# Kernel optimization log

Hardware: AMD Instinct MI355X
Metric: run time of the kernel (lower is better)

## Reference

```python
import jax, jax.numpy as jnp
import numpy as np

B, C, H, W = 4, 8, 384, 384
NUM_LAYERS = 5
CG_ITERS = 10


def conv2d(x, w, b):
    # x: [B,Cin,H,W], w: [Cout,Cin,3,3]
    y = jax.lax.conv_general_dilated(x, w, (1, 1), 'SAME',
                                     dimension_numbers=('NCHW', 'OIHW', 'NCHW'))
    return y + b[None, :, None, None]


def dw(x, w_in, b_in, ws_mid, bs_mid, w_out, b_out):
    # Sequence: conv, conv, relu, conv, conv, relu, conv, conv, relu, conv, conv, relu, conv
    h = conv2d(x, w_in, b_in)
    for i in range(7):
        h = conv2d(h, ws_mid[i], bs_mid[i])
        if i % 2 == 0:  # ReLU after convs 2,4,6,8
            h = jax.nn.relu(h)
    h = conv2d(h, w_out, b_out)
    return x + h  # residual


def conjugate_grad(rhs, csm_c, mask, lam):
    # rhs: [B,H,W] complex; csm_c: [B,C,H,W] complex; mask: [B,H,W] real
    def AtA(p):
        coil = csm_c * p[:, None]                      # [B,C,H,W]
        k = jnp.fft.fft2(coil) * mask[:, None]         # masked k-space
        return jnp.sum(jnp.conj(csm_c) * jnp.fft.ifft2(k), axis=1)

    def body(carry, _):
        x, r, p, rTr = carry
        Ap = AtA(p) + lam * p
        pAp = jnp.sum(jnp.conj(p) * Ap, axis=(-2, -1)).real
        alpha = rTr / pAp
        x = x + alpha[:, None, None] * p
        r = r - alpha[:, None, None] * Ap
        rTrNew = jnp.sum(jnp.conj(r) * r, axis=(-2, -1)).real
        beta = rTrNew / rTr
        p = r + beta[:, None, None] * p
        return (x, r, p, rTrNew), None

    x0 = jnp.zeros_like(rhs)
    rTr0 = jnp.sum(jnp.conj(rhs) * rhs, axis=(-2, -1)).real
    (x, _, _, _), _ = jax.lax.scan(body, (x0, rhs, rhs, rTr0), None, length=CG_ITERS)
    return x


def reference(under_img, csm, mask, lam, w_in, b_in, ws_mid, bs_mid, w_out, b_out):
    csm_c = jax.lax.complex(csm[..., 0], csm[..., 1])  # [B,C,H,W] complex
    lam_s = lam[0]
    x = under_img
    for _ in range(NUM_LAYERS):
        x = dw(x, w_in, b_in, ws_mid, bs_mid, w_out, b_out)
        x = under_img + lam_s * x
        rhs = jax.lax.complex(x[:, 0], x[:, 1])        # view_as_complex(permute(0,2,3,1))
        xc = conjugate_grad(rhs, csm_c, mask, lam_s)
        x = jnp.stack([xc.real, xc.imag], axis=1)      # view_as_real -> [B,2,H,W]
    return x


def setup_inputs() -> dict:
    key = jax.random.key(0)
    ks = jax.random.split(key, 8)
    under_img = jax.random.normal(ks[0], (B, 2, H, W), jnp.float32)
    csm = jax.random.normal(ks[1], (B, C, H, W, 2), jnp.float32) / np.sqrt(C)
    mask = (jax.random.uniform(ks[2], (B, H, W)) > 0.5).astype(jnp.float32)
    lam = jnp.array([0.05], jnp.float32)
    w_in = jax.random.normal(ks[3], (64, 2, 3, 3), jnp.float32) * 0.02
    b_in = jnp.zeros((64,), jnp.float32)
    ws_mid = jax.random.normal(ks[4], (7, 64, 64, 3, 3), jnp.float32) * 0.02
    bs_mid = jnp.zeros((7, 64), jnp.float32)
    w_out = jax.random.normal(ks[5], (2, 64, 3, 3), jnp.float32) * 0.02
    b_out = jnp.zeros((2,), jnp.float32)
    return {"under_img": under_img, "csm": csm, "mask": mask, "lam": lam,
            "w_in": w_in, "b_in": b_in, "ws_mid": ws_mid, "bs_mid": bs_mid,
            "w_out": w_out, "b_out": b_out}
```

## Files before the change

kernel.cpp:

```cpp
#include <hip/hip_runtime.h>
#include <hip/hip_bf16.h>
#include <math.h>

#define HH 384
#define WW 384
#define HW (HH*WW)
#define WP 386
#define PP (386*386)
#define BB 4
#define CC 8
#define NLAYERS 5
#define CGITERS 10
#define PI_F 3.14159265358979323846f

typedef __attribute__((ext_vector_type(8))) short short8;
typedef __attribute__((ext_vector_type(4))) float floatx4;

struct cf { float x, y; };
__device__ __forceinline__ cf cadd(cf a, cf b){ cf r; r.x=a.x+b.x; r.y=a.y+b.y; return r; }
__device__ __forceinline__ cf csub(cf a, cf b){ cf r; r.x=a.x-b.x; r.y=a.y-b.y; return r; }
__device__ __forceinline__ cf cmul(cf a, cf b){ cf r; r.x=a.x*b.x - a.y*b.y; r.y=a.x*b.y + a.y*b.x; return r; }
__device__ __forceinline__ cf csqr(cf a){ cf r; r.x = a.x*a.x - a.y*a.y; r.y = 2.f*a.x*a.y; return r; }
__device__ __forceinline__ cf shflxor(cf v, int m){ cf r; r.x = __shfl_xor(v.x, m); r.y = __shfl_xor(v.y, m); return r; }
__device__ __forceinline__ int brev7(int l){ return (int)(__brev((unsigned)l) >> 25); }
__device__ __forceinline__ int padi(int i){ return i + (i >> 3); }

__device__ __forceinline__ void radix3(cf a0, cf a1, cf a2, float s3, cf y[3]) {
  float tx = a1.x + a2.x, ty_ = a1.y + a2.y;
  float ux = a1.x - a2.x, uy = a1.y - a2.y;
  y[0].x = a0.x + tx;              y[0].y = a0.y + ty_;
  y[1].x = a0.x - 0.5f*tx - s3*uy; y[1].y = a0.y - 0.5f*ty_ + s3*ux;
  y[2].x = a0.x - 0.5f*tx + s3*uy; y[2].y = a0.y - 0.5f*ty_ - s3*ux;
}

template<int SIGN>
__device__ __forceinline__ void fft384_wave(int l, const cf v[6], cf uA[3], cf uB[3]) {
  const float s3 = SIGN * 0.8660254037844386f;
  radix3(v[0], v[2], v[4], s3, uA);
  radix3(v[1], v[3], v[5], s3, uB);
  float sA, cA;
  __sincosf(SIGN * (2.0f * PI_F / 384.0f) * (float)l, &sA, &cA);
  cf wA1; wA1.x = cA; wA1.y = sA;
  cf wA2 = csqr(wA1);
  cf w6; w6.x = 0.5f; w6.y = s3;
  cf wB1 = cmul(wA1, w6);
  cf wB2 = csqr(wB1);
  uA[1] = cmul(uA[1], wA1); uA[2] = cmul(uA[2], wA2);
  uB[1] = cmul(uB[1], wB1); uB[2] = cmul(uB[2], wB2);
  cf u = cmul(wA2, wA1);
  #pragma unroll
  for (int k1 = 0; k1 < 3; ++k1) {
    cf a = uA[k1], b = uB[k1];
    uA[k1] = cadd(a, b);
    uB[k1] = cmul(csub(a, b), u);
  }
  #pragma unroll
  for (int h = 32; h >= 1; h >>= 1) {
    u = csqr(u);
    const bool up = (l & h) != 0;
    #pragma unroll
    for (int k1 = 0; k1 < 3; ++k1) {
      cf pa = shflxor(uA[k1], h);
      cf pb = shflxor(uB[k1], h);
      cf na = up ? cmul(csub(uA[k1], pa), u) : cadd(uA[k1], pa);
      cf nb = up ? cmul(csub(uB[k1], pb), u) : cadd(uB[k1], pb);
      uA[k1] = na; uB[k1] = nb;
    }
  }
}


__global__ void repack_mid_k(const float* __restrict__ ws_mid, __hip_bfloat16* __restrict__ wrep) {
  const int idx = blockIdx.x * 256 + threadIdx.x;
  if (idx >= 7*9*64*64) return;
  const int ci = idx & 63, co = (idx >> 6) & 63, tap = (idx >> 12) % 9, i = idx / (9*4096);
  wrep[idx] = __float2bfloat16(ws_mid[(((size_t)i*64 + co)*64 + ci)*9 + tap]);
}

__global__ void zero_guard_k(__hip_bfloat16* __restrict__ a, __hip_bfloat16* __restrict__ b2) {
  const int idx = blockIdx.x * 256 + threadIdx.x;
  if (idx >= 2*BB*1540*8) return;
  const int s = idx & 7; int rest = idx >> 3;
  const int px = rest % 1540; rest /= 1540;
  const int bb = rest & 3; const int buf = rest >> 2;
  int row, col;
  if (px < WP)        { row = 0;    col = px; }
  else if (px < 2*WP) { row = HH+1; col = px - WP; }
  else { const int k = px - 2*WP; row = 1 + (k >> 1); col = (k & 1) ? (WW+1) : 0; }
  __hip_bfloat16* base = buf ? b2 : a;
  *(uint4*)(base + ((size_t)bb*PP + (size_t)row*WP + col)*64 + s*8) = make_uint4(0u,0u,0u,0u);
}

__global__ void __launch_bounds__(256) conv_in_k(const float* __restrict__ xin,
                                                 const float* __restrict__ w,
                                                 const float* __restrict__ bias,
                                                 __hip_bfloat16* __restrict__ out) {
  __shared__ float tile[2][340];
  const int tx = threadIdx.x & 31, ty = threadIdx.x >> 5;
  const int x0 = blockIdx.x * 32, y0 = blockIdx.y * 8, b = blockIdx.z;
  for (int e = threadIdx.x; e < 680; e += 256) {
    int ci = e / 340, rr = e % 340;
    int iy = y0 - 1 + rr / 34, ix = x0 - 1 + rr % 34;
    float v = 0.f;
    if (iy >= 0 && iy < HH && ix >= 0 && ix < WW)
      v = xin[(b*2 + ci)*HW + iy*WW + ix];
    tile[ci][rr] = v;
  }
  __syncthreads();
  float acc[64];
  #pragma unroll
  for (int co = 0; co < 64; ++co) acc[co] = bias[co];
  #pragma unroll
  for (int ci = 0; ci < 2; ++ci) {
    float v0 = tile[ci][ty*34+tx],     v1 = tile[ci][ty*34+tx+1],     v2 = tile[ci][ty*34+tx+2];
    float v3 = tile[ci][(ty+1)*34+tx], v4 = tile[ci][(ty+1)*34+tx+1], v5 = tile[ci][(ty+1)*34+tx+2];
    float v6 = tile[ci][(ty+2)*34+tx], v7 = tile[ci][(ty+2)*34+tx+1], v8 = tile[ci][(ty+2)*34+tx+2];
    #pragma unroll
    for (int co = 0; co < 64; ++co) {
      const float* wp = w + co*18 + ci*9;
      float a = acc[co];
      a = fmaf(v0, wp[0], a); a = fmaf(v1, wp[1], a); a = fmaf(v2, wp[2], a);
      a = fmaf(v3, wp[3], a); a = fmaf(v4, wp[4], a); a = fmaf(v5, wp[5], a);
      a = fmaf(v6, wp[6], a); a = fmaf(v7, wp[7], a); a = fmaf(v8, wp[8], a);
      acc[co] = a;
    }
  }
  const size_t obase = ((size_t)b*PP + (size_t)(y0 + ty + 1)*WP + (x0 + tx + 1))*64;
  #pragma unroll
  for (int s = 0; s < 8; ++s) {
    uint4 u;
    __hip_bfloat16* hp = (__hip_bfloat16*)&u;
    #pragma unroll
    for (int j = 0; j < 8; ++j) hp[j] = __float2bfloat16(acc[s*8 + j]);
    *(uint4*)(out + obase + s*8) = u;
  }
}

__global__ void __launch_bounds__(512, 4) conv_mid_mfma_k(
    const __hip_bfloat16* __restrict__ in,
    const __hip_bfloat16* __restrict__ wrep,
    const float* __restrict__ bias,
    __hip_bfloat16* __restrict__ out, int relu) {
  __shared__ __align__(16) __hip_bfloat16 atile[612*64];
  const int tid = threadIdx.x;
  const int l = tid & 63, wv = tid >> 6;
  const int x0 = blockIdx.x * 32, y0 = blockIdx.y * 16, b = blockIdx.z;

  const int kseg = l >> 4;
  const int lr = l & 15;

  const __hip_bfloat16* wlane = wrep + lr*64 + kseg*8;
  short8 bf[4][2];
  #pragma unroll
  for (int nt = 0; nt < 4; ++nt) {
    bf[nt][0] = *(const short8*)(wlane + nt*1024);
    bf[nt][1] = *(const short8*)(wlane + nt*1024 + 32);
  }

  const __hip_bfloat16* inb = in + (size_t)b*PP*64;
  #pragma unroll
  for (int i = 0; i < 9; ++i) {
    const int j = i*512 + tid;
    const int p = j >> 3, s = j & 7;
    const int g = s ^ (p & 7);
    const __hip_bfloat16* src = inb + ((size_t)(y0 + p/34)*WP + (x0 + p%34))*64 + g*8;
    __builtin_amdgcn_global_load_lds(
        (const __attribute__((address_space(1))) void*)src,
        (__attribute__((address_space(3))) void*)(atile + (i*512 + wv*64)*8),
        16, 0, 0);
  }
  if (tid < 288) {
    const int j = 4608 + tid;
    const int p = j >> 3, s = j & 7;
    const int g = s ^ (p & 7);
    uint4 v = *(const uint4*)(inb + ((size_t)(y0 + p/34)*WP + (x0 + p%34))*64 + g*8);
    *(uint4*)(atile + (size_t)j*8) = v;
  }

  floatx4 acc[4][4];
  #pragma unroll
  for (int mt = 0; mt < 4; ++mt)
    #pragma unroll
    for (int nt = 0; nt < 4; ++nt)
      acc[mt][nt] = (floatx4){0.f, 0.f, 0.f, 0.f};

  __syncthreads();

  #pragma unroll 1
  for (int tap = 0; tap < 9; ++tap) {
    short8 bfn[4][2];
    if (tap < 8) {
      const __hip_bfloat16* wn = wlane + (tap + 1)*4096;
      #pragma unroll
      for (int nt = 0; nt < 4; ++nt) {
        bfn[nt][0] = *(const short8*)(wn + nt*1024);
        bfn[nt][1] = *(const short8*)(wn + nt*1024 + 32);
      }
    }
    const int dy = tap / 3, dx = tap - dy*3;
    short8 af[4][2];
    #pragma unroll
    for (int mt = 0; mt < 4; ++mt) {
      const int ry = 2*wv + (mt >> 1) + dy;
      const int px = (mt & 1)*16 + lr + dx;
      const int p  = ry*34 + px;
      const int eo = p*64 + ((kseg ^ (p & 7)) << 3);
      af[mt][0] = *(const short8*)(atile + eo);
      af[mt][1] = *(const short8*)(atile + (eo ^ 32));
    }
    #pragma unroll
    for (int mt = 0; mt < 4; ++mt)
      #pragma unroll
      for (int nt = 0; nt < 4; ++nt) {
        acc[mt][nt] = __builtin_amdgcn_mfma_f32_16x16x32_bf16(af[mt][0], bf[nt][0], acc[mt][nt], 0, 0, 0);
        acc[mt][nt] = __builtin_amdgcn_mfma_f32_16x16x32_bf16(af[mt][1], bf[nt][1], acc[mt][nt], 0, 0, 0);
      }
    if (tap < 8) {
      #pragma unroll
      for (int nt = 0; nt < 4; ++nt) { bf[nt][0] = bfn[nt][0]; bf[nt][1] = bfn[nt][1]; }
    }
  }

  __syncthreads();
  __hip_bfloat16* otile = atile;
  #pragma unroll
  for (int mt = 0; mt < 4; ++mt) {
    const int row = 2*wv + (mt >> 1);
    #pragma unroll
    for (int nt = 0; nt < 4; ++nt) {
      const int ch = nt*16 + lr;
      const float bv = bias[ch];
      #pragma unroll
      for (int rr = 0; rr < 4; ++rr) {
        const int px = (mt & 1)*16 + kseg*4 + rr;
        float v = acc[mt][nt][rr] + bv;
        if (relu) v = fmaxf(v, 0.f);
        otile[(row*32 + px)*72 + ch] = __float2bfloat16(v);
      }
    }
  }
  __syncthreads();
  #pragma unroll
  for (int iter = 0; iter < 8; ++iter) {
    const int p = iter*64 + (tid >> 3), s = tid & 7;
    const int row = p >> 5, px = p & 31;
    uint4 v = *(const uint4*)(&otile[p*72 + s*8]);
    *(uint4*)(out + ((size_t)b*PP + (size_t)(y0 + row + 1)*WP + (x0 + px + 1))*64 + s*8) = v;
  }
}

__global__ void __launch_bounds__(256) conv_out_k(const __hip_bfloat16* __restrict__ in,
                                                  const float* __restrict__ w,
                                                  const float* __restrict__ bias,
                                                  const float* __restrict__ xcur,
                                                  const float* __restrict__ under,
                                                  const float* __restrict__ lam,
                                                  cf* __restrict__ r, cf* __restrict__ p,
                                                  cf* __restrict__ xc, float* __restrict__ scL) {
  __shared__ __hip_bfloat16 atile[340*72];
  __shared__ float wl[2*64*9];
  __shared__ float wsum[4];
  const int tid = threadIdx.x;
  const int tx = tid & 31, ty = tid >> 5;
  const int x0 = blockIdx.x * 32, y0 = blockIdx.y * 8, b = blockIdx.z;

  for (int e = tid; e < 340*8; e += 256) {
    int pp = e >> 3, s = e & 7;
    uint4 v = *(const uint4*)(in + ((size_t)b*PP + (size_t)(y0 + pp/34)*WP + (x0 + pp%34))*64 + s*8);
    *(uint4*)(&atile[pp*72 + s*8]) = v;
  }
  for (int e = tid; e < 2*64*9; e += 256) wl[e] = w[e];
  __syncthreads();

  float a0 = bias[0], a1 = bias[1];
  #pragma unroll 1
  for (int tap = 0; tap < 9; ++tap) {
    const int dy = tap / 3, dx = tap - dy*3;
    const __hip_bfloat16* ap = &atile[((ty + dy)*34 + tx + dx)*72];
    #pragma unroll
    for (int s = 0; s < 8; ++s) {
      short8 v8 = *(const short8*)(ap + s*8);
      const __hip_bfloat16* hv = (const __hip_bfloat16*)&v8;
      #pragma unroll
      for (int j = 0; j < 8; ++j) {
        const float f = __bfloat162float(hv[j]);
        a0 = fmaf(f, wl[(s*8 + j)*9 + tap], a0);
        a1 = fmaf(f, wl[(64 + s*8 + j)*9 + tap], a1);
      }
    }
  }
  const float lamv = lam[0];
  const int y = y0 + ty, x = x0 + tx;
  const int idx2 = y*WW + x;
  float xv0 = xcur[b*2*HW + idx2],  xv1 = xcur[b*2*HW + HW + idx2];
  float u0  = under[b*2*HW + idx2], u1  = under[b*2*HW + HW + idx2];
  float r0 = u0 + lamv * (xv0 + a0);
  float r1 = u1 + lamv * (xv1 + a1);
  const int cidx = b*HW + idx2;
  cf vv; vv.x = r0; vv.y = r1;
  r[cidx] = vv; p[cidx] = vv;
  cf zz; zz.x = 0.f; zz.y = 0.f; xc[cidx] = zz;
  float partial = r0*r0 + r1*r1;
  for (int off = 32; off; off >>= 1) partial += __shfl_down(partial, off);
  const int l = tid & 63, wvid = tid >> 6;
  if (l == 0) wsum[wvid] = partial;
  __syncthreads();
  if (tid == 0) atomicAdd(&scL[b], wsum[0]+wsum[1]+wsum[2]+wsum[3]);
}


__global__ void __launch_bounds__(256) pass_a_k(const cf* __restrict__ rold, cf* __restrict__ rnew,
                                                const cf* __restrict__ pold, cf* __restrict__ pnew,
                                                cf* __restrict__ xc, const cf* __restrict__ Ap,
                                                const cf* __restrict__ csm, cf* __restrict__ t,
                                                float* __restrict__ scL, int it) {
  __shared__ cf rowbuf[4][434];
  const int l = threadIdx.x & 63, wv = threadIdx.x >> 6;
  const int y = blockIdx.x * 4 + wv;
  const int c = blockIdx.y, b = blockIdx.z;
  const int rowoff = b*HW + y*WW;
  cf pv[6];
  if (it == 0) {
    #pragma unroll
    for (int m = 0; m < 6; ++m) pv[m] = pold[rowoff + l + 64*m];
  } else {
    const float rtrp  = scL[(it-1)*4 + b];
    const float pApp  = scL[40 + (it-1)*4 + b];
    const float ApApp = scL[80 + (it-1)*4 + b];
    const float alpha = rtrp / pApp;
    const float rtrn  = alpha*alpha*ApApp - rtrp;
    const float beta  = rtrn / rtrp;
    if (blockIdx.x == 0 && c == 0 && threadIdx.x == 0) scL[it*4 + b] = rtrn;
    #pragma unroll
    for (int m = 0; m < 6; ++m) {
      const int idx = rowoff + l + 64*m;
      cf rv = rold[idx];
      cf av = Ap[idx];
      rv.x -= alpha*av.x; rv.y -= alpha*av.y;
      cf po = pold[idx];
      pv[m].x = rv.x + beta*po.x; pv[m].y = rv.y + beta*po.y;
      if (c == 0) {
        rnew[idx] = rv;
        pnew[idx] = pv[m];
        cf xv = xc[idx]; xv.x += alpha*po.x; xv.y += alpha*po.y; xc[idx] = xv;
      }
    }
  }
  const cf* crow = csm + (b*CC + c)*HW + y*WW;
  cf v[6];
  #pragma unroll
  for (int m = 0; m < 6; ++m) v[m] = cmul(crow[l + 64*m], pv[m]);
  cf uA[3], uB[3];
  fft384_wave<-1>(l, v, uA, uB);
  const int R3 = 3 * brev7(l);
  cf* rb = rowbuf[wv];
  #pragma unroll
  for (int k1 = 0; k1 < 3; ++k1) { rb[padi(k1 + R3)] = uA[k1]; rb[padi(k1 + R3 + 3)] = uB[k1]; }
  cf* trow = t + (b*CC + c)*HW + y*WW;
  #pragma unroll
  for (int m = 0; m < 6; ++m) trow[l + 64*m] = rb[padi(l + 64*m)];
}

__global__ void __launch_bounds__(256) pass_b_k(cf* __restrict__ t, const float* __restrict__ mask) {
  __shared__ cf tile[431*9];
  const int b = blockIdx.z, c = blockIdx.y, x0 = blockIdx.x * 8;
  cf* base = t + (b*CC + c)*HW;
  for (int e = threadIdx.x; e < 3072; e += 256) {
    int y = e >> 3, xx = e & 7;
    tile[padi(y)*9 + xx] = base[y*WW + x0 + xx];
  }
  __syncthreads();
  const int l = threadIdx.x & 63, wv = threadIdx.x >> 6;
  const int R3 = 3 * brev7(l);
  for (int rep = 0; rep < 2; ++rep) {
    const int xx = wv*2 + rep, x = x0 + xx;
    cf v[6];
    #pragma unroll
    for (int m = 0; m < 6; ++m) v[m] = tile[padi(l + 64*m)*9 + xx];
    cf uA[3], uB[3];
    fft384_wave<-1>(l, v, uA, uB);
    const float* mrow = mask + b*HW + x;
    #pragma unroll
    for (int k1 = 0; k1 < 3; ++k1) {
      float mA = mrow[(k1 + R3)*WW], mB = mrow[(k1 + R3 + 3)*WW];
      uA[k1].x *= mA; uA[k1].y *= mA; uB[k1].x *= mB; uB[k1].y *= mB;
    }
    __syncthreads();
    #pragma unroll
    for (int k1 = 0; k1 < 3; ++k1) { tile[padi(k1 + R3)*9 + xx] = uA[k1]; tile[padi(k1 + R3 + 3)*9 + xx] = uB[k1]; }
    __syncthreads();
    #pragma unroll
    for (int m = 0; m < 6; ++m) v[m] = tile[padi(l + 64*m)*9 + xx];
    fft384_wave<1>(l, v, uA, uB);
    const float s = 1.0f / 384.0f;
    #pragma unroll
    for (int k1 = 0; k1 < 3; ++k1) {
      uA[k1].x *= s; uA[k1].y *= s; uB[k1].x *= s; uB[k1].y *= s;
      tile[padi(k1 + R3)*9 + xx] = uA[k1]; tile[padi(k1 + R3 + 3)*9 + xx] = uB[k1];
    }
    __syncthreads();
  }
  for (int e = threadIdx.x; e < 3072; e += 256) {
    int y = e >> 3, xx = e & 7;
    base[y*WW + x0 + xx] = tile[padi(y)*9 + xx];
  }
}

__global__ void __launch_bounds__(256) pass_c_k(const cf* __restrict__ t, const cf* __restrict__ csm,
                                                const cf* __restrict__ p, cf* __restrict__ Ap,
                                                const float* __restrict__ lam,
                                                float* __restrict__ scL, int it) {
  __shared__ cf rowbuf[4][434];
  __shared__ cf redbuf[3][384];
  const int l = threadIdx.x & 63, wv = threadIdx.x >> 6;
  const int y = blockIdx.x, b = blockIdx.y;
  const int R3 = 3 * brev7(l);
  cf* rb = rowbuf[wv];
  cf acc[6] = {};
  #pragma unroll 1
  for (int ci = 0; ci < 2; ++ci) {
    const int c = wv*2 + ci;
    const cf* trow = t + (b*CC + c)*HW + y*WW;
    cf v[6];
    #pragma unroll
    for (int m = 0; m < 6; ++m) v[m] = trow[l + 64*m];
    cf uA[3], uB[3];
    fft384_wave<1>(l, v, uA, uB);
    #pragma unroll
    for (int k1 = 0; k1 < 3; ++k1) { rb[padi(k1 + R3)] = uA[k1]; rb[padi(k1 + R3 + 3)] = uB[k1]; }
    const cf* crow = csm + (b*CC + c)*HW + y*WW;
    #pragma unroll
    for (int m = 0; m < 6; ++m) {
      cf cs = crow[l + 64*m];
      cf wz = rb[padi(l + 64*m)];
      acc[m].x += cs.x*wz.x + cs.y*wz.y;
      acc[m].y += cs.x*wz.y - cs.y*wz.x;
    }
  }
  if (wv > 0) {
    #pragma unroll
    for (int m = 0; m < 6; ++m) redbuf[wv - 1][l + 64*m] = acc[m];
  }
  __syncthreads();
  if (wv == 0) {
    #pragma unroll
    for (int m = 0; m < 6; ++m) {
      #pragma unroll
      for (int j = 0; j < 3; ++j) {
        cf o = redbuf[j][l + 64*m];
        acc[m].x += o.x; acc[m].y += o.y;
      }
    }
    const float lamv = lam[0];
    const float sc384 = 1.0f / 384.0f;
    const cf* prow = p + b*HW + y*WW;
    cf* aprow = Ap + b*HW + y*WW;
    float partial = 0.f, partial2 = 0.f;
    #pragma unroll
    for (int m = 0; m < 6; ++m) {
      cf pv = prow[l + 64*m];
      cf ap; ap.x = acc[m].x*sc384 + lamv*pv.x; ap.y = acc[m].y*sc384 + lamv*pv.y;
      aprow[l + 64*m] = ap;
      partial  += pv.x*ap.x + pv.y*ap.y;
      partial2 += ap.x*ap.x + ap.y*ap.y;
    }
    #pragma unroll
    for (int off = 32; off; off >>= 1) {
      partial  += __shfl_down(partial, off);
      partial2 += __shfl_down(partial2, off);
    }
    if (l == 0) {
      atomicAdd(&scL[40 + it*4 + b], partial);
      atomicAdd(&scL[80 + it*4 + b], partial2);
    }
  }
}

__global__ void __launch_bounds__(256) final_x_k(const cf* __restrict__ xc, const cf* __restrict__ p9,
                                                 const float* __restrict__ scL, float* __restrict__ out) {
  const int idx = blockIdx.x * 256 + threadIdx.x;
  const int b = idx / HW;
  const int rem = idx - b*HW;
  const float alpha = scL[(CGITERS-1)*4 + b] / scL[40 + (CGITERS-1)*4 + b];
  cf xv = xc[idx], pv = p9[idx];
  xv.x += alpha*pv.x; xv.y += alpha*pv.y;
  out[b*2*HW + rem] = xv.x;
  out[b*2*HW + HW + rem] = xv.y;
}

__global__ void zero_sc_k(float* sc) {
  for (int i = threadIdx.x; i < NLAYERS*128; i += 256) sc[i] = 0.f;
}

extern "C" void kernel_launch(void* const* d_in, const int* in_sizes, int n_in,
                              void* d_out, int out_size, void* d_ws, size_t ws_size,
                              hipStream_t stream) {
  (void)in_sizes; (void)n_in; (void)out_size; (void)ws_size;
  const float* under  = (const float*)d_in[0];
  const cf*    csm    = (const cf*)d_in[1];
  const float* mask   = (const float*)d_in[2];
  const float* lam    = (const float*)d_in[3];
  const float* w_in   = (const float*)d_in[4];
  const float* b_in   = (const float*)d_in[5];
  const float* ws_mid = (const float*)d_in[6];
  const float* bs_mid = (const float*)d_in[7];
  const float* w_out  = (const float*)d_in[8];
  const float* b_out  = (const float*)d_in[9];
  float* xcur = (float*)d_out;

  char* bws = (char*)d_ws;
  size_t off = 0;
  auto carve = [&](size_t bytes) { char* pp = bws + off; off += (bytes + 255) & ~(size_t)255; return (void*)pp; };
  __hip_bfloat16* actA = (__hip_bfloat16*)carve((size_t)BB*PP*64*2);
  __hip_bfloat16* actB = (__hip_bfloat16*)carve((size_t)BB*PP*64*2);
  cf* t     = (cf*)carve((size_t)BB*CC*HW*8);
  cf* rbuf0 = (cf*)carve((size_t)BB*HW*8);
  cf* rbuf1 = (cf*)carve((size_t)BB*HW*8);
  cf* pbuf0 = (cf*)carve((size_t)BB*HW*8);
  cf* pbuf1 = (cf*)carve((size_t)BB*HW*8);
  cf* xc    = (cf*)carve((size_t)BB*HW*8);
  cf* Ap    = (cf*)carve((size_t)BB*HW*8);
  float* sc = (float*)carve(4096);
  __hip_bfloat16* wrep = (__hip_bfloat16*)carve((size_t)7*9*64*64*2);

  hipMemcpyAsync(xcur, under, (size_t)BB*2*HW*sizeof(float), hipMemcpyDeviceToDevice, stream);

  zero_sc_k<<<1, 256, 0, stream>>>(sc);
  repack_mid_k<<<(7*9*64*64 + 255)/256, 256, 0, stream>>>(ws_mid, wrep);
  zero_guard_k<<<(2*BB*1540*8 + 255)/256, 256, 0, stream>>>(actA, actB);

  dim3 cgrid(WW/32, HH/8, BB);
  dim3 cmgrid(WW/32, HH/16, BB);
  dim3 agrid(HH/4, CC, BB);
  dim3 bgrid(WW/8, CC, BB);
  dim3 c2grid(HH, BB);
  const int egrid = BB*HW/256;

  __hip_bfloat16* bufs[2] = { actA, actB };
  cf* rb[2] = { rbuf0, rbuf1 };
  cf* pb[2] = { pbuf0, pbuf1 };

  for (int layer = 0; layer < NLAYERS; ++layer) {
    float* scL = sc + layer*128;
    conv_in_k<<<cgrid, 256, 0, stream>>>(xcur, w_in, b_in, bufs[0]);
    for (int i = 0; i < 7; ++i) {
      conv_mid_mfma_k<<<cmgrid, 512, 0, stream>>>(bufs[i & 1], wrep + (size_t)i*9*4096,
                                                  bs_mid + i*64, bufs[(i + 1) & 1], (i % 2 == 0) ? 1 : 0);
    }
    conv_out_k<<<cgrid, 256, 0, stream>>>(bufs[1], w_out, b_out, xcur, under, lam,
                                          rbuf0, pbuf0, xc, scL);
    for (int it = 0; it < CGITERS; ++it) {
      cf* rold = rb[(it + 1) & 1];
      cf* rnew = rb[it & 1];
      cf* pold = pb[(it + 1) & 1];
      cf* pnew = pb[it & 1];
      if (it == 0) { rold = rbuf0; pold = pbuf0; rnew = rbuf0; pnew = pbuf0; }
      pass_a_k<<<agrid, 256, 0, stream>>>(rold, rnew, pold, pnew, xc, Ap, csm, t, scL, it);
      pass_b_k<<<bgrid, 256, 0, stream>>>(t, mask);
      pass_c_k<<<c2grid, 256, 0, stream>>>(t, csm, pnew, Ap, lam, scL, it);
    }
    final_x_k<<<egrid, 256, 0, stream>>>(xc, pb[(CGITERS - 1) & 1], scL, xcur);
  }
}
```

Baseline: 10.86 ms.

## Make mid conv persistent with double-buffered async LDS tile prefetch

Converts the 64-channel MFMA conv into a persistent kernel over 256 blocks, each looping over tiles. The next tile's input halo is prefetched into a second LDS buffer with global_load_lds while the current tile runs, gated by explicit vmcnt waits and barriers. The aim is to hide global load latency behind MFMA work and cut launch and tail effects. In exchange LDS per block doubles, the occupancy hint drops from 4 to 2, and weights are reloaded on every tile.

```diff
diff --git a/kernel.cpp b/kernel.cpp
--- a/kernel.cpp
+++ b/kernel.cpp
@@ -136,116 +136,153 @@
   }
 }
 
-__global__ void __launch_bounds__(512, 4) conv_mid_mfma_k(
+__global__ void __launch_bounds__(512, 2) conv_mid_mfma_k(
     const __hip_bfloat16* __restrict__ in,
     const __hip_bfloat16* __restrict__ wrep,
     const float* __restrict__ bias,
     __hip_bfloat16* __restrict__ out, int relu) {
-  __shared__ __align__(16) __hip_bfloat16 atile[612*64];
+  __shared__ __align__(16) __hip_bfloat16 atile[2][4928*8];
   const int tid = threadIdx.x;
   const int l = tid & 63, wv = tid >> 6;
-  const int x0 = blockIdx.x * 32, y0 = blockIdx.y * 16, b = blockIdx.z;
-
   const int kseg = l >> 4;
   const int lr = l & 15;
-
   const __hip_bfloat16* wlane = wrep + lr*64 + kseg*8;
-  short8 bf[4][2];
-  #pragma unroll
-  for (int nt = 0; nt < 4; ++nt) {
-    bf[nt][0] = *(const short8*)(wlane + nt*1024);
-    bf[nt][1] = *(const short8*)(wlane + nt*1024 + 32);
-  }
-
-  const __hip_bfloat16* inb = in + (size_t)b*PP*64;
-  #pragma unroll
-  for (int i = 0; i < 9; ++i) {
-    const int j = i*512 + tid;
-    const int p = j >> 3, s = j & 7;
-    const int g = s ^ (p & 7);
-    const __hip_bfloat16* src = inb + ((size_t)(y0 + p/34)*WP + (x0 + p%34))*64 + g*8;
-    __builtin_amdgcn_global_load_lds(
-        (const __attribute__((address_space(1))) void*)src,
-        (__attribute__((address_space(3))) void*)(atile + (i*512 + wv*64)*8),
-        16, 0, 0);
-  }
-  if (tid < 288) {
-    const int j = 4608 + tid;
-    const int p = j >> 3, s = j & 7;
-    const int g = s ^ (p & 7);
-    uint4 v = *(const uint4*)(inb + ((size_t)(y0 + p/34)*WP + (x0 + p%34))*64 + g*8);
-    *(uint4*)(atile + (size_t)j*8) = v;
-  }
-
-  floatx4 acc[4][4];
-  #pragma unroll
-  for (int mt = 0; mt < 4; ++mt)
-    #pragma unroll
-    for (int nt = 0; nt < 4; ++nt)
-      acc[mt][nt] = (floatx4){0.f, 0.f, 0.f, 0.f};
-
-  __syncthreads();
+
+  const int NT = 12*24*4;
+
+  auto stage = [&](int bi, int tt) {
+    const int tx_ = tt % 12, ty_ = (tt / 12) % 24, b = tt / 288;
+    const int x0 = tx_ * 32, y0 = ty_ * 16;
+    const __hip_bfloat16* inb = in + (size_t)b*PP*64;
+    __hip_bfloat16* A = &atile[bi][0];
+    #pragma unroll
+    for (int i = 0; i < 9; ++i) {
+      const int j = i*512 + tid;
+      const int p = j >> 3, s = j & 7;
+      const int g = s ^ (p & 7);
+      const __hip_bfloat16* src = inb + ((size_t)(y0 + p/34)*WP + (x0 + p%34))*64 + g*8;
+      __builtin_amdgcn_global_load_lds(
+          (const __attribute__((address_space(1))) void*)src,
+          (__attribute__((address_space(3))) void*)(A + (i*512 + wv*64)*8),
+          16, 0, 0);
+    }
+    if (tid < 288) {
+      const int j = 4608 + tid;
+      const int jj = j < 4896 ? j : 4895;
+      const int p = jj >> 3, s = jj & 7;
+      const int g = s ^ (p & 7);
+      const __hip_bfloat16* src = inb + ((size_t)(y0 + p/34)*WP + (x0 + p%34))*64 + g*8;
+      __builtin_amdgcn_global_load_lds(
+          (const __attribute__((address_space(1))) void*)src,
+          (__attribute__((address_space(3))) void*)(A + (4608 + wv*64)*8),
+          16, 0, 0);
+    }
+  };
+
+  int t = blockIdx.x;
+  int cur = 0;
+  stage(cur, t);
 
   #pragma unroll 1
-  for (int tap = 0; tap < 9; ++tap) {
-    short8 bfn[4][2];
-    if (tap < 8) {
-      const __hip_bfloat16* wn = wlane + (tap + 1)*4096;
+  for (; t < NT; t += 256) {
+    const int tx_ = t % 12, ty_ = (t / 12) % 24, b = t / 288;
+    const int x0 = tx_ * 32, y0 = ty_ * 16;
+    const bool more = (t + 256) < NT;
+    if (more) stage(cur ^ 1, t + 256);
+
+    if (more) {
+      if (wv < 5) asm volatile("s_waitcnt vmcnt(10)" ::: "memory");
+      else        asm volatile("s_waitcnt vmcnt(9)"  ::: "memory");
+    } else {
+      asm volatile("s_waitcnt vmcnt(0)" ::: "memory");
+    }
+    __builtin_amdgcn_s_barrier();
+    __builtin_amdgcn_sched_barrier(0);
+
+    const __hip_bfloat16* A = &atile[cur][0];
+
+    short8 bf[4][2];
+    #pragma unroll
+    for (int nt = 0; nt < 4; ++nt) {
+      bf[nt][0] = *(const short8*)(wlane + nt*1024);
+      bf[nt][1] = *(const short8*)(wlane + nt*1024 + 32);
+    }
+
+    floatx4 acc[4][4];
+    #pragma unroll
+    for (int mt = 0; mt < 4; ++mt)
+      #pragma unroll
+      for (int nt = 0; nt < 4; ++nt)
+        acc[mt][nt] = (floatx4){0.f, 0.f, 0.f, 0.f};
+
+    #pragma unroll 1
+    for (int tap = 0; tap < 9; ++tap) {
+      short8 bfn[4][2];
+      if (tap < 8) {
+        const __hip_bfloat16* wn = wlane + (tap + 1)*4096;
+        #pragma unroll
+        for (int nt = 0; nt < 4; ++nt) {
+          bfn[nt][0] = *(const short8*)(wn + nt*1024);
+          bfn[nt][1] = *(const short8*)(wn + nt*1024 + 32);
+        }
+      }
+      const int dy = tap / 3, dx = tap - dy*3;
+      short8 af[4][2];
+      #pragma unroll
+      for (int mt = 0; mt < 4; ++mt) {
+        const int ry = 2*wv + (mt >> 1) + dy;
+        const int px = (mt & 1)*16 + lr + dx;
+        const int p  = ry*34 + px;
+        const int eo = p*64 + ((kseg ^ (p & 7)) << 3);
+        af[mt][0] = *(const short8*)(A + eo);
+        af[mt][1] = *(const short8*)(A + (eo ^ 32));
+      }
+      #pragma unroll
+      for (int mt = 0; mt < 4; ++mt)
+        #pragma unroll
+        for (int nt = 0; nt < 4; ++nt) {
+          acc[mt][nt] = __builtin_amdgcn_mfma_f32_16x16x32_bf16(af[mt][0], bf[nt][0], acc[mt][nt], 0, 0, 0);
+          acc[mt][nt] = __builtin_amdgcn_mfma_f32_16x16x32_bf16(af[mt][1], bf[nt][1], acc[mt][nt], 0, 0, 0);
+        }
+      if (tap < 8) {
+        #pragma unroll
+        for (int nt = 0; nt < 4; ++nt) { bf[nt][0] = bfn[nt][0]; bf[nt][1] = bfn[nt][1]; }
+      }
+    }
+
+    asm volatile("s_waitcnt lgkmcnt(0)" ::: "memory");
+    __builtin_amdgcn_s_barrier();
+
+    __hip_bfloat16* otile = &atile[cur][0];
+    #pragma unroll
+    for (int mt = 0; mt < 4; ++mt) {
+      const int row = 2*wv + (mt >> 1);
       #pragma unroll
       for (int nt = 0; nt < 4; ++nt) {
-        bfn[nt][0] = *(const short8*)(wn + nt*1024);
-        bfn[nt][1] = *(const short8*)(wn + nt*1024 + 32);
+        const int ch = nt*16 + lr;
+        const float bv = bias[ch];
+        #pragma unroll
+        for (int rr = 0; rr < 4; ++rr) {
+          const int px = (mt & 1)*16 + kseg*4 + rr;
+          float v = acc[mt][nt][rr] + bv;
+          if (relu) v = fmaxf(v, 0.f);
+          otile[(row*32 + px)*72 + ch] = __float2bfloat16(v);
+        }
       }
     }
-    const int dy = tap / 3, dx = tap - dy*3;
-    short8 af[4][2];
-    #pragma unroll
-    for (int mt = 0; mt < 4; ++mt) {
-      const int ry = 2*wv + (mt >> 1) + dy;
-      const int px = (mt & 1)*16 + lr + dx;
-      const int p  = ry*34 + px;
-      const int eo = p*64 + ((kseg ^ (p & 7)) << 3);
-      af[mt][0] = *(const short8*)(atile + eo);
-      af[mt][1] = *(const short8*)(atile + (eo ^ 32));
-    }
-    #pragma unroll
-    for (int mt = 0; mt < 4; ++mt)
-      #pragma unroll
-      for (int nt = 0; nt < 4; ++nt) {
-        acc[mt][nt] = __builtin_amdgcn_mfma_f32_16x16x32_bf16(af[mt][0], bf[nt][0], acc[mt][nt], 0, 0, 0);
-        acc[mt][nt] = __builtin_amdgcn_mfma_f32_16x16x32_bf16(af[mt][1], bf[nt][1], acc[mt][nt], 0, 0, 0);
-      }
-    if (tap < 8) {
-      #pragma unroll
-      for (int nt = 0; nt < 4; ++nt) { bf[nt][0] = bfn[nt][0]; bf[nt][1] = bfn[nt][1]; }
-    }
-  }
-
-  __syncthreads();
-  __hip_bfloat16* otile = atile;
-  #pragma unroll
-  for (int mt = 0; mt < 4; ++mt) {
-    const int row = 2*wv + (mt >> 1);
-    #pragma unroll
-    for (int nt = 0; nt < 4; ++nt) {
-      const int ch = nt*16 + lr;
-      const float bv = bias[ch];
-      #pragma unroll
-      for (int rr = 0; rr < 4; ++rr) {
-        const int px = (mt & 1)*16 + kseg*4 + rr;
-        float v = acc[mt][nt][rr] + bv;
-        if (relu) v = fmaxf(v, 0.f);
-        otile[(row*32 + px)*72 + ch] = __float2bfloat16(v);
-      }
-    }
-  }
-  __syncthreads();
-  #pragma unroll
-  for (int iter = 0; iter < 8; ++iter) {
-    const int p = iter*64 + (tid >> 3), s = tid & 7;
-    const int row = p >> 5, px = p & 31;
-    uint4 v = *(const uint4*)(&otile[p*72 + s*8]);
-    *(uint4*)(out + ((size_t)b*PP + (size_t)(y0 + row + 1)*WP + (x0 + px + 1))*64 + s*8) = v;
+    asm volatile("s_waitcnt lgkmcnt(0)" ::: "memory");
+    __builtin_amdgcn_s_barrier();
+    #pragma unroll
+    for (int iter = 0; iter < 8; ++iter) {
+      const int p = iter*64 + (tid >> 3), s = tid & 7;
+      const int row = p >> 5, px = p & 31;
+      uint4 v = *(const uint4*)(&otile[p*72 + s*8]);
+      *(uint4*)(out + ((size_t)b*PP + (size_t)(y0 + row + 1)*WP + (x0 + px + 1))*64 + s*8) = v;
+    }
+    asm volatile("s_waitcnt lgkmcnt(0)" ::: "memory");
+    __builtin_amdgcn_s_barrier();
+
+    cur ^= 1;
   }
 }
 
@@ -530,7 +567,6 @@
   zero_guard_k<<<(2*BB*1540*8 + 255)/256, 256, 0, stream>>>(actA, actB);
 
   dim3 cgrid(WW/32, HH/8, BB);
-  dim3 cmgrid(WW/32, HH/16, BB);
   dim3 agrid(HH/4, CC, BB);
   dim3 bgrid(WW/8, CC, BB);
   dim3 c2grid(HH, BB);
@@ -544,8 +580,8 @@
     float* scL = sc + layer*128;
     conv_in_k<<<cgrid, 256, 0, stream>>>(xcur, w_in, b_in, bufs[0]);
     for (int i = 0; i < 7; ++i) {
-      conv_mid_mfma_k<<<cmgrid, 512, 0, stream>>>(bufs[i & 1], wrep + (size_t)i*9*4096,
-                                                  bs_mid + i*64, bufs[(i + 1) & 1], (i % 2 == 0) ? 1 : 0);
+      conv_mid_mfma_k<<<dim3(256), 512, 0, stream>>>(bufs[i & 1], wrep + (size_t)i*9*4096,
+                                                     bs_mid + i*64, bufs[(i + 1) & 1], (i % 2 == 0) ? 1 : 0);
     }
     conv_out_k<<<cgrid, 256, 0, stream>>>(bufs[1], w_out, b_out, xcur, under, lam,
                                           rbuf0, pbuf0, xc, scL);
```

Result: faster. 10.05 ms (-7.4%).

## Shrink conv tiles, split CG update into separate kernel, parallelize pass_c reduction

Applied to the files above, without the earlier changes.

The mid conv kernel now uses 256-thread blocks over 8-row tiles instead of 512 threads over 16 rows, which halves LDS per block and doubles the grid. The CG vector update moves out of pass_a_k into a separate elementwise update_k, so pass_a_k's eight per-coil blocks no longer each recompute the r/p update. pass_c_k now spreads its final cross-wave reduction over all four waves instead of funnelling it through wave 0. These changes cost an extra kernel launch plus an extra read and write of p per CG iteration, and more halo reloads in the conv.

```diff
diff --git a/kernel.cpp b/kernel.cpp
--- a/kernel.cpp
+++ b/kernel.cpp
@@ -136,15 +136,15 @@
   }
 }
 
-__global__ void __launch_bounds__(512, 4) conv_mid_mfma_k(
+__global__ void __launch_bounds__(256) conv_mid_mfma_k(
     const __hip_bfloat16* __restrict__ in,
     const __hip_bfloat16* __restrict__ wrep,
     const float* __restrict__ bias,
     __hip_bfloat16* __restrict__ out, int relu) {
-  __shared__ __align__(16) __hip_bfloat16 atile[612*64];
+  __shared__ __align__(16) __hip_bfloat16 atile[2752*8];
   const int tid = threadIdx.x;
   const int l = tid & 63, wv = tid >> 6;
-  const int x0 = blockIdx.x * 32, y0 = blockIdx.y * 16, b = blockIdx.z;
+  const int x0 = blockIdx.x * 32, y0 = blockIdx.y * 8, b = blockIdx.z;
 
   const int kseg = l >> 4;
   const int lr = l & 15;
@@ -159,22 +159,22 @@
 
   const __hip_bfloat16* inb = in + (size_t)b*PP*64;
   #pragma unroll
-  for (int i = 0; i < 9; ++i) {
-    const int j = i*512 + tid;
+  for (int i = 0; i < 10; ++i) {
+    const int j = i*256 + tid;
     const int p = j >> 3, s = j & 7;
     const int g = s ^ (p & 7);
     const __hip_bfloat16* src = inb + ((size_t)(y0 + p/34)*WP + (x0 + p%34))*64 + g*8;
     __builtin_amdgcn_global_load_lds(
         (const __attribute__((address_space(1))) void*)src,
-        (__attribute__((address_space(3))) void*)(atile + (i*512 + wv*64)*8),
+        (__attribute__((address_space(3))) void*)(atile + (i*256 + wv*64)*8),
         16, 0, 0);
   }
-  if (tid < 288) {
-    const int j = 4608 + tid;
+  if (tid < 160) {
+    const int j = 2560 + tid;
     const int p = j >> 3, s = j & 7;
     const int g = s ^ (p & 7);
     uint4 v = *(const uint4*)(inb + ((size_t)(y0 + p/34)*WP + (x0 + p%34))*64 + g*8);
-    *(uint4*)(atile + (size_t)j*8) = v;
+    *(uint4*)(atile + j*8) = v;
   }
 
   floatx4 acc[4][4];
@@ -242,7 +242,7 @@
   __syncthreads();
   #pragma unroll
   for (int iter = 0; iter < 8; ++iter) {
-    const int p = iter*64 + (tid >> 3), s = tid & 7;
+    const int p = iter*32 + (tid >> 3), s = tid & 7;
     const int row = p >> 5, px = p & 31;
     uint4 v = *(const uint4*)(&otile[p*72 + s*8]);
     *(uint4*)(out + ((size_t)b*PP + (size_t)(y0 + row + 1)*WP + (x0 + px + 1))*64 + s*8) = v;
@@ -309,47 +309,40 @@
 }
 
 
-__global__ void __launch_bounds__(256) pass_a_k(const cf* __restrict__ rold, cf* __restrict__ rnew,
+__global__ void __launch_bounds__(256) update_k(const cf* __restrict__ rold, cf* __restrict__ rnew,
                                                 const cf* __restrict__ pold, cf* __restrict__ pnew,
                                                 cf* __restrict__ xc, const cf* __restrict__ Ap,
-                                                const cf* __restrict__ csm, cf* __restrict__ t,
                                                 float* __restrict__ scL, int it) {
+  const int idx = blockIdx.x * 256 + threadIdx.x;
+  const int b = idx / HW;
+  const float rtrp  = scL[(it-1)*4 + b];
+  const float pApp  = scL[40 + (it-1)*4 + b];
+  const float ApApp = scL[80 + (it-1)*4 + b];
+  const float alpha = rtrp / pApp;
+  const float rtrn  = alpha*alpha*ApApp - rtrp;
+  const float beta  = rtrn / rtrp;
+  if ((idx - b*HW) == 0) scL[it*4 + b] = rtrn;
+  cf rv = rold[idx];
+  cf av = Ap[idx];
+  rv.x -= alpha*av.x; rv.y -= alpha*av.y;
+  cf po = pold[idx];
+  cf pv; pv.x = rv.x + beta*po.x; pv.y = rv.y + beta*po.y;
+  rnew[idx] = rv;
+  pnew[idx] = pv;
+  cf xv = xc[idx]; xv.x += alpha*po.x; xv.y += alpha*po.y; xc[idx] = xv;
+}
+
+__global__ void __launch_bounds__(256) pass_a_k(const cf* __restrict__ pin,
+                                                const cf* __restrict__ csm, cf* __restrict__ t) {
   __shared__ cf rowbuf[4][434];
   const int l = threadIdx.x & 63, wv = threadIdx.x >> 6;
   const int y = blockIdx.x * 4 + wv;
   const int c = blockIdx.y, b = blockIdx.z;
-  const int rowoff = b*HW + y*WW;
-  cf pv[6];
-  if (it == 0) {
-    #pragma unroll
-    for (int m = 0; m < 6; ++m) pv[m] = pold[rowoff + l + 64*m];
-  } else {
-    const float rtrp  = scL[(it-1)*4 + b];
-    const float pApp  = scL[40 + (it-1)*4 + b];
-    const float ApApp = scL[80 + (it-1)*4 + b];
-    const float alpha = rtrp / pApp;
-    const float rtrn  = alpha*alpha*ApApp - rtrp;
-    const float beta  = rtrn / rtrp;
-    if (blockIdx.x == 0 && c == 0 && threadIdx.x == 0) scL[it*4 + b] = rtrn;
-    #pragma unroll
-    for (int m = 0; m < 6; ++m) {
-      const int idx = rowoff + l + 64*m;
-      cf rv = rold[idx];
-      cf av = Ap[idx];
-      rv.x -= alpha*av.x; rv.y -= alpha*av.y;
-      cf po = pold[idx];
-      pv[m].x = rv.x + beta*po.x; pv[m].y = rv.y + beta*po.y;
-      if (c == 0) {
-        rnew[idx] = rv;
-        pnew[idx] = pv[m];
-        cf xv = xc[idx]; xv.x += alpha*po.x; xv.y += alpha*po.y; xc[idx] = xv;
-      }
-    }
-  }
+  const cf* prow = pin + b*HW + y*WW;
   const cf* crow = csm + (b*CC + c)*HW + y*WW;
   cf v[6];
   #pragma unroll
-  for (int m = 0; m < 6; ++m) v[m] = cmul(crow[l + 64*m], pv[m]);
+  for (int m = 0; m < 6; ++m) v[m] = cmul(crow[l + 64*m], prow[l + 64*m]);
   cf uA[3], uB[3];
   fft384_wave<-1>(l, v, uA, uB);
   const int R3 = 3 * brev7(l);
@@ -410,14 +403,15 @@
                                                 const cf* __restrict__ p, cf* __restrict__ Ap,
                                                 const float* __restrict__ lam,
                                                 float* __restrict__ scL, int it) {
-  __shared__ cf rowbuf[4][434];
-  __shared__ cf redbuf[3][384];
-  const int l = threadIdx.x & 63, wv = threadIdx.x >> 6;
+  __shared__ cf rowbuf[4][2][434];
+  __shared__ cf redbuf[4][384];
+  __shared__ float wsums[4][2];
+  const int tid = threadIdx.x;
+  const int l = tid & 63, wv = tid >> 6;
   const int y = blockIdx.x, b = blockIdx.y;
   const int R3 = 3 * brev7(l);
-  cf* rb = rowbuf[wv];
   cf acc[6] = {};
-  #pragma unroll 1
+  #pragma unroll
   for (int ci = 0; ci < 2; ++ci) {
     const int c = wv*2 + ci;
     const cf* trow = t + (b*CC + c)*HW + y*WW;
@@ -426,6 +420,7 @@
     for (int m = 0; m < 6; ++m) v[m] = trow[l + 64*m];
     cf uA[3], uB[3];
     fft384_wave<1>(l, v, uA, uB);
+    cf* rb = rowbuf[wv][ci];
     #pragma unroll
     for (int k1 = 0; k1 < 3; ++k1) { rb[padi(k1 + R3)] = uA[k1]; rb[padi(k1 + R3 + 3)] = uB[k1]; }
     const cf* crow = csm + (b*CC + c)*HW + y*WW;
@@ -437,42 +432,38 @@
       acc[m].y += cs.x*wz.y - cs.y*wz.x;
     }
   }
-  if (wv > 0) {
-    #pragma unroll
-    for (int m = 0; m < 6; ++m) redbuf[wv - 1][l + 64*m] = acc[m];
-  }
-  __syncthreads();
-  if (wv == 0) {
-    #pragma unroll
-    for (int m = 0; m < 6; ++m) {
-      #pragma unroll
-      for (int j = 0; j < 3; ++j) {
-        cf o = redbuf[j][l + 64*m];
-        acc[m].x += o.x; acc[m].y += o.y;
-      }
-    }
-    const float lamv = lam[0];
-    const float sc384 = 1.0f / 384.0f;
-    const cf* prow = p + b*HW + y*WW;
-    cf* aprow = Ap + b*HW + y*WW;
-    float partial = 0.f, partial2 = 0.f;
-    #pragma unroll
-    for (int m = 0; m < 6; ++m) {
-      cf pv = prow[l + 64*m];
-      cf ap; ap.x = acc[m].x*sc384 + lamv*pv.x; ap.y = acc[m].y*sc384 + lamv*pv.y;
-      aprow[l + 64*m] = ap;
+  #pragma unroll
+  for (int m = 0; m < 6; ++m) redbuf[wv][m*64 + l] = acc[m];
+  __syncthreads();
+
+  const float lamv = lam[0];
+  const float sc384 = 1.0f / 384.0f;
+  const cf* prow = p + b*HW + y*WW;
+  cf* aprow = Ap + b*HW + y*WW;
+  float partial = 0.f, partial2 = 0.f;
+  #pragma unroll
+  for (int rep = 0; rep < 2; ++rep) {
+    const int pos = rep*256 + tid;
+    if (pos < 384) {
+      cf s0 = redbuf[0][pos], s1 = redbuf[1][pos], s2 = redbuf[2][pos], s3 = redbuf[3][pos];
+      cf s; s.x = (s0.x + s1.x) + (s2.x + s3.x); s.y = (s0.y + s1.y) + (s2.y + s3.y);
+      cf pv = prow[pos];
+      cf ap; ap.x = s.x*sc384 + lamv*pv.x; ap.y = s.y*sc384 + lamv*pv.y;
+      aprow[pos] = ap;
       partial  += pv.x*ap.x + pv.y*ap.y;
       partial2 += ap.x*ap.x + ap.y*ap.y;
     }
-    #pragma unroll
-    for (int off = 32; off; off >>= 1) {
-      partial  += __shfl_down(partial, off);
-      partial2 += __shfl_down(partial2, off);
-    }
-    if (l == 0) {
-      atomicAdd(&scL[40 + it*4 + b], partial);
-      atomicAdd(&scL[80 + it*4 + b], partial2);
-    }
+  }
+  #pragma unroll
+  for (int off = 32; off; off >>= 1) {
+    partial  += __shfl_down(partial, off);
+    partial2 += __shfl_down(partial2, off);
+  }
+  if (l == 0) { wsums[wv][0] = partial; wsums[wv][1] = partial2; }
+  __syncthreads();
+  if (tid == 0) {
+    atomicAdd(&scL[40 + it*4 + b], (wsums[0][0]+wsums[1][0])+(wsums[2][0]+wsums[3][0]));
+    atomicAdd(&scL[80 + it*4 + b], (wsums[0][1]+wsums[1][1])+(wsums[2][1]+wsums[3][1]));
   }
 }
 
@@ -530,7 +521,6 @@
   zero_guard_k<<<(2*BB*1540*8 + 255)/256, 256, 0, stream>>>(actA, actB);
 
   dim3 cgrid(WW/32, HH/8, BB);
-  dim3 cmgrid(WW/32, HH/16, BB);
   dim3 agrid(HH/4, CC, BB);
   dim3 bgrid(WW/8, CC, BB);
   dim3 c2grid(HH, BB);
@@ -544,8 +534,8 @@
     float* scL = sc + layer*128;
     conv_in_k<<<cgrid, 256, 0, stream>>>(xcur, w_in, b_in, bufs[0]);
     for (int i = 0; i < 7; ++i) {
-      conv_mid_mfma_k<<<cmgrid, 512, 0, stream>>>(bufs[i & 1], wrep + (size_t)i*9*4096,
-                                                  bs_mid + i*64, bufs[(i + 1) & 1], (i % 2 == 0) ? 1 : 0);
+      conv_mid_mfma_k<<<cgrid, 256, 0, stream>>>(bufs[i & 1], wrep + (size_t)i*9*4096,
+                                                 bs_mid + i*64, bufs[(i + 1) & 1], (i % 2 == 0) ? 1 : 0);
     }
     conv_out_k<<<cgrid, 256, 0, stream>>>(bufs[1], w_out, b_out, xcur, under, lam,
                                           rbuf0, pbuf0, xc, scL);
@@ -555,7 +545,9 @@
       cf* pold = pb[(it + 1) & 1];
       cf* pnew = pb[it & 1];
       if (it == 0) { rold = rbuf0; pold = pbuf0; rnew = rbuf0; pnew = pbuf0; }
-      pass_a_k<<<agrid, 256, 0, stream>>>(rold, rnew, pold, pnew, xc, Ap, csm, t, scL, it);
+      if (it > 0)
+        update_k<<<egrid, 256, 0, stream>>>(rold, rnew, pold, pnew, xc, Ap, scL, it);
+      pass_a_k<<<agrid, 256, 0, stream>>>(pnew, csm, t);
       pass_b_k<<<bgrid, 256, 0, stream>>>(t, mask);
       pass_c_k<<<c2grid, 256, 0, stream>>>(t, csm, pnew, Ap, lam, scL, it);
     }
```

Result: faster. 9.423 ms (-13.2%).
